# Optimization experiments

Measured on AMD Instinct MI355X. Metric: run time of the kernel, lower is better.

## Reference

```python
import jax, jax.numpy as jnp
import numpy as np

N_NODES = 200_000
N_EDGES = 12_800_000


def setup_inputs() -> dict:
    key = jax.random.key(0)
    k1, k2, k3, k4 = jax.random.split(key, 4)
    x = jax.random.normal(k1, (N_NODES, 2), dtype=jnp.float32)
    edge_index = jax.random.randint(k2, (2, N_EDGES), 0, N_NODES, dtype=jnp.int32)
    # Glorot-ish init for the two GCN linear layers
    W1 = jax.random.normal(k3, (2, 16), dtype=jnp.float32) * 0.5
    b1 = jnp.zeros((16,), dtype=jnp.float32)
    W2 = jax.random.normal(k4, (16, 2), dtype=jnp.float32) * 0.25
    b2 = jnp.zeros((2,), dtype=jnp.float32)
    return {"x": x, "W1": W1, "b1": b1, "W2": W2, "b2": b2, "edge_index": edge_index}


def gcn_conv(x, W, b, src, dst, num_nodes):
    # PyG GCNConv: add self-loops, deg from dst (col), norm = d_src^-1/2 * d_dst^-1/2,
    # out[i] = sum_{j->i} norm_e * (x_j W) + (1/deg_i) * (x_i W) + b
    h = x @ W  # [N, F_out]
    ones = jnp.ones(src.shape[0], dtype=h.dtype)
    deg = jax.ops.segment_sum(ones, dst, num_segments=num_nodes) + 1.0  # +1 self-loop
    dinv = jax.lax.rsqrt(deg)  # [N]
    norm = dinv[src] * dinv[dst]  # [E]
    agg = jax.ops.segment_sum(h[src] * norm[:, None], dst, num_segments=num_nodes)
    # self-loop contribution has norm dinv_i * dinv_i = 1/deg_i
    return agg + h * (1.0 / deg)[:, None] + b


def reference(x, W1, b1, W2, b2, edge_index):
    src, dst = edge_index[0], edge_index[1]
    h = gcn_conv(x, W1, b1, src, dst, N_NODES)
    h = jax.nn.relu(h)
    out = gcn_conv(h, W2, b2, src, dst, N_NODES)
    return out
```

## Files before the change

kernel.cpp:

```cpp
#include <hip/hip_runtime.h>


constexpr int N_NODES = 200000;
constexpr int N_EDGES = 12800000;
constexpr int RANGE_SHIFT = 8;
constexpr int K_BUCKETS = (N_NODES + 255) / 256;
constexpr int SORT_BLOCKS = 2048;
constexpr int CHUNK = N_EDGES / SORT_BLOCKS;
constexpr int SCAN_R = SORT_BLOCKS / 256;
constexpr int SEG = 4;


__global__ __launch_bounds__(256) void hist_kernel(const int* __restrict__ dst,
                                                   unsigned* __restrict__ blockHist) {
    __shared__ unsigned h[K_BUCKETS];
    for (int i = threadIdx.x; i < K_BUCKETS; i += 256) h[i] = 0;
    __syncthreads();
    int base = blockIdx.x * CHUNK;
    for (int e = base + threadIdx.x; e < base + CHUNK; e += 256)
        atomicAdd(&h[((unsigned)dst[e]) >> RANGE_SHIFT], 1u);
    __syncthreads();
    unsigned* row = blockHist + (size_t)blockIdx.x * K_BUCKETS;
    for (int i = threadIdx.x; i < K_BUCKETS; i += 256) row[i] = h[i];
}

__global__ __launch_bounds__(256) void scan_perblock_kernel(unsigned* __restrict__ blockHist,
                                                            unsigned* __restrict__ bucketTotal) {
    int b = blockIdx.x, t = threadIdx.x;
    unsigned v[SCAN_R], run = 0;
#pragma unroll
    for (int j = 0; j < SCAN_R; j++) v[j] = blockHist[(size_t)(SCAN_R * t + j) * K_BUCKETS + b];
#pragma unroll
    for (int j = 0; j < SCAN_R; j++) { unsigned tmp = v[j]; v[j] = run; run += tmp; }
    __shared__ unsigned sh[256];
    sh[t] = run;
    __syncthreads();
    for (int off = 1; off < 256; off <<= 1) {
        unsigned add = (t >= off) ? sh[t - off] : 0u;
        __syncthreads();
        sh[t] += add;
        __syncthreads();
    }
    unsigned excl = sh[t] - run;
#pragma unroll
    for (int j = 0; j < SCAN_R; j++)
        blockHist[(size_t)(SCAN_R * t + j) * K_BUCKETS + b] = excl + v[j];
    if (t == 255) bucketTotal[b] = sh[255];
}

__global__ __launch_bounds__(1024) void scan_buckets_kernel(const unsigned* __restrict__ bucketTotal,
                                                            unsigned* __restrict__ bucketStart) {
    __shared__ unsigned sh[1024];
    int t = threadIdx.x;
    unsigned v = (t < K_BUCKETS) ? bucketTotal[t] : 0u;
    sh[t] = v;
    __syncthreads();
    for (int off = 1; off < 1024; off <<= 1) {
        unsigned add = (t >= off) ? sh[t - off] : 0u;
        __syncthreads();
        sh[t] += add;
        __syncthreads();
    }
    if (t < K_BUCKETS) bucketStart[t] = sh[t] - v;
    if (t == K_BUCKETS - 1) bucketStart[K_BUCKETS] = sh[t];
}

__global__ __launch_bounds__(256) void scatter_kernel(const int* __restrict__ src,
                                                      const int* __restrict__ dst,
                                                      const unsigned* __restrict__ blockHist,
                                                      const unsigned* __restrict__ bucketStart,
                                                      unsigned* __restrict__ sorted) {
    __shared__ unsigned s_hist[K_BUCKETS];
    __shared__ unsigned s_cur[K_BUCKETS];
    __shared__ int      s_base[K_BUCKETS];
    __shared__ unsigned ssum[256];
    __shared__ unsigned ent[CHUNK];
    __shared__ unsigned short bk[CHUNK];

    int t = threadIdx.x;
    int base = blockIdx.x * CHUNK;
    for (int i = t; i < K_BUCKETS; i += 256) s_hist[i] = 0;
    __syncthreads();

    for (int e = base + t; e < base + CHUNK; e += 256)
        atomicAdd(&s_hist[((unsigned)dst[e]) >> RANGE_SHIFT], 1u);
    __syncthreads();

    unsigned v[4], run = 0;
#pragma unroll
    for (int j = 0; j < 4; j++) {
        int idx = 4 * t + j;
        v[j] = (idx < K_BUCKETS) ? s_hist[idx] : 0u;
    }
#pragma unroll
    for (int j = 0; j < 4; j++) { unsigned tmp = v[j]; v[j] = run; run += tmp; }
    ssum[t] = run;
    __syncthreads();
    for (int off = 1; off < 256; off <<= 1) {
        unsigned add = (t >= off) ? ssum[t - off] : 0u;
        __syncthreads();
        ssum[t] += add;
        __syncthreads();
    }
    unsigned excl = ssum[t] - run;
    const unsigned* row = blockHist + (size_t)blockIdx.x * K_BUCKETS;
#pragma unroll
    for (int j = 0; j < 4; j++) {
        int idx = 4 * t + j;
        if (idx < K_BUCKETS) {
            unsigned st = excl + v[j];
            s_cur[idx] = st;
            s_base[idx] = (int)(bucketStart[idx] + row[idx]) - (int)st;
        }
    }
    __syncthreads();

    for (int e = base + t; e < base + CHUNK; e += 256) {
        unsigned d = (unsigned)dst[e];
        unsigned s = (unsigned)src[e];
        unsigned b = d >> RANGE_SHIFT;
        unsigned lpos = atomicAdd(&s_cur[b], 1u);
        ent[lpos] = s | ((d & 255u) << 18);
        bk[lpos] = (unsigned short)b;
    }
    __syncthreads();

    for (int i = t; i < CHUNK; i += 256) {
        unsigned b = bk[i];
        sorted[s_base[b] + i] = ent[i];
    }
}


__global__ __launch_bounds__(256) void deg_part_kernel(const unsigned* __restrict__ sorted,
                                                       const unsigned* __restrict__ bucketStart,
                                                       unsigned* __restrict__ pcnt) {
    __shared__ unsigned cnt[256];
    int t = threadIdx.x;
    cnt[t] = 0;
    __syncthreads();
    int b = blockIdx.x >> 2, s = blockIdx.x & 3;
    int s0 = bucketStart[b], len = bucketStart[b + 1] - s0;
    int e0 = s0 + (len * s) / SEG;
    int e1 = s0 + (len * (s + 1)) / SEG;
    int e = e0 + t;
    for (; e < e1 - 768; e += 1024) {
        unsigned w0 = sorted[e], w1 = sorted[e + 256], w2 = sorted[e + 512], w3 = sorted[e + 768];
        atomicAdd(&cnt[(w0 >> 18) & 255u], 1u);
        atomicAdd(&cnt[(w1 >> 18) & 255u], 1u);
        atomicAdd(&cnt[(w2 >> 18) & 255u], 1u);
        atomicAdd(&cnt[(w3 >> 18) & 255u], 1u);
    }
    for (; e < e1; e += 256)
        atomicAdd(&cnt[(sorted[e] >> 18) & 255u], 1u);
    __syncthreads();
    pcnt[(size_t)blockIdx.x * 256 + t] = cnt[t];
}

__global__ __launch_bounds__(256) void node1_kernel(const float2* __restrict__ x,
                                                    const unsigned* __restrict__ pcnt,
                                                    float* __restrict__ dinv,
                                                    float2* __restrict__ u) {
    int i = blockIdx.x * 256 + threadIdx.x;
    if (i >= N_NODES) return;
    int b = i >> 8, l = i & 255;
    unsigned c = 1;
#pragma unroll
    for (int s = 0; s < SEG; s++) c += pcnt[(size_t)(b * SEG + s) * 256 + l];
    float di = rsqrtf((float)c);
    dinv[i] = di;
    float2 xi = x[i];
    u[i] = make_float2(di * xi.x, di * xi.y);
}

__global__ __launch_bounds__(256) void agg_part_kernel(const unsigned* __restrict__ sorted,
                                                       const unsigned* __restrict__ bucketStart,
                                                       const float2* __restrict__ table,
                                                       float2* __restrict__ part) {
    __shared__ float ax[256], ay[256];
    int t = threadIdx.x;
    ax[t] = 0.f; ay[t] = 0.f;
    __syncthreads();
    int b = blockIdx.x >> 2, s = blockIdx.x & 3;
    int s0 = bucketStart[b], len = bucketStart[b + 1] - s0;
    int e0 = s0 + (len * s) / SEG;
    int e1 = s0 + (len * (s + 1)) / SEG;
    int e = e0 + t;
    for (; e < e1 - 768; e += 1024) {
        unsigned w0 = sorted[e], w1 = sorted[e + 256], w2 = sorted[e + 512], w3 = sorted[e + 768];
        float2 v0 = table[w0 & 0x3FFFFu];
        float2 v1 = table[w1 & 0x3FFFFu];
        float2 v2 = table[w2 & 0x3FFFFu];
        float2 v3 = table[w3 & 0x3FFFFu];
        atomicAdd(&ax[(w0 >> 18) & 255u], v0.x); atomicAdd(&ay[(w0 >> 18) & 255u], v0.y);
        atomicAdd(&ax[(w1 >> 18) & 255u], v1.x); atomicAdd(&ay[(w1 >> 18) & 255u], v1.y);
        atomicAdd(&ax[(w2 >> 18) & 255u], v2.x); atomicAdd(&ay[(w2 >> 18) & 255u], v2.y);
        atomicAdd(&ax[(w3 >> 18) & 255u], v3.x); atomicAdd(&ay[(w3 >> 18) & 255u], v3.y);
    }
    for (; e < e1; e += 256) {
        unsigned w = sorted[e];
        float2 v = table[w & 0x3FFFFu];
        unsigned l = (w >> 18) & 255u;
        atomicAdd(&ax[l], v.x);
        atomicAdd(&ay[l], v.y);
    }
    __syncthreads();
    part[(size_t)blockIdx.x * 256 + t] = make_float2(ax[t], ay[t]);
}

__global__ __launch_bounds__(256) void node2_kernel(const float2* __restrict__ u,
                                                    const float2* __restrict__ part,
                                                    const float* __restrict__ W1,
                                                    const float* __restrict__ b1,
                                                    const float* __restrict__ W2,
                                                    const float* __restrict__ dinv,
                                                    float2* __restrict__ g2) {
    int i = blockIdx.x * 256 + threadIdx.x;
    if (i >= N_NODES) return;
    int b = i >> 8, l = i & 255;
    float ax = 0.f, ay = 0.f;
#pragma unroll
    for (int s = 0; s < SEG; s++) {
        float2 p = part[(size_t)(b * SEG + s) * 256 + l];
        ax += p.x; ay += p.y;
    }
    float di = dinv[i];
    float2 uu = u[i];
    float c0 = di * (ax + uu.x);
    float c1 = di * (ay + uu.y);
    float a0 = 0.f, a1 = 0.f;
#pragma unroll
    for (int f = 0; f < 16; f++) {
        float o = fmaxf(c0 * W1[f] + c1 * W1[16 + f] + b1[f], 0.f);
        a0 += o * W2[2 * f];
        a1 += o * W2[2 * f + 1];
    }
    g2[i] = make_float2(di * a0, di * a1);
}

__global__ __launch_bounds__(256) void node3_kernel(const float2* __restrict__ g2,
                                                    const float2* __restrict__ part,
                                                    const float* __restrict__ b2,
                                                    const float* __restrict__ dinv,
                                                    float2* __restrict__ out) {
    int i = blockIdx.x * 256 + threadIdx.x;
    if (i >= N_NODES) return;
    int b = i >> 8, l = i & 255;
    float ax = 0.f, ay = 0.f;
#pragma unroll
    for (int s = 0; s < SEG; s++) {
        float2 p = part[(size_t)(b * SEG + s) * 256 + l];
        ax += p.x; ay += p.y;
    }
    float di = dinv[i];
    float2 g = g2[i];
    out[i] = make_float2(di * (ax + g.x) + b2[0],
                         di * (ay + g.y) + b2[1]);
}


__global__ __launch_bounds__(256) void fb_deg(const int* __restrict__ dst, int* __restrict__ degi) {
    int e = blockIdx.x * 256 + threadIdx.x;
    if (e < N_EDGES) atomicAdd(&degi[dst[e]], 1);
}
__global__ __launch_bounds__(256) void fb_node1(const float* __restrict__ x, const int* __restrict__ degi,
                                                float* __restrict__ dinv, float2* __restrict__ u) {
    int i = blockIdx.x * 256 + threadIdx.x;
    if (i >= N_NODES) return;
    float di = rsqrtf((float)(degi[i] + 1));
    dinv[i] = di;
    float2 xi = ((const float2*)x)[i];
    u[i] = make_float2(di * xi.x, di * xi.y);
}
__global__ __launch_bounds__(256) void fb_agg(const int* __restrict__ src, const int* __restrict__ dst,
                                              const float2* __restrict__ table, float* __restrict__ acc) {
    int e = blockIdx.x * 256 + threadIdx.x;
    if (e >= N_EDGES) return;
    float2 v = table[src[e]];
    size_t d = dst[e];
    unsafeAtomicAdd(&acc[2 * d], v.x);
    unsafeAtomicAdd(&acc[2 * d + 1], v.y);
}
__global__ __launch_bounds__(256) void fb_node2(const float2* __restrict__ u, const float2* __restrict__ A1,
                                                const float* __restrict__ W1, const float* __restrict__ b1,
                                                const float* __restrict__ W2, const float* __restrict__ dinv,
                                                float2* __restrict__ g2) {
    int i = blockIdx.x * 256 + threadIdx.x;
    if (i >= N_NODES) return;
    float di = dinv[i];
    float2 a = A1[i], uu = u[i];
    float c0 = di * (a.x + uu.x), c1 = di * (a.y + uu.y);
    float a0 = 0.f, a1 = 0.f;
#pragma unroll
    for (int f = 0; f < 16; f++) {
        float o = fmaxf(c0 * W1[f] + c1 * W1[16 + f] + b1[f], 0.f);
        a0 += o * W2[2 * f];
        a1 += o * W2[2 * f + 1];
    }
    g2[i] = make_float2(di * a0, di * a1);
}
__global__ __launch_bounds__(256) void fb_node3(const float2* __restrict__ g2, const float2* __restrict__ A2,
                                                const float* __restrict__ b2, const float* __restrict__ dinv,
                                                float2* __restrict__ out) {
    int i = blockIdx.x * 256 + threadIdx.x;
    if (i >= N_NODES) return;
    float di = dinv[i];
    float2 a = A2[i], g = g2[i];
    out[i] = make_float2(di * (a.x + g.x) + b2[0], di * (a.y + g.y) + b2[1]);
}


extern "C" void kernel_launch(void* const* d_in, const int* in_sizes, int n_in,
                              void* d_out, int out_size, void* d_ws, size_t ws_size,
                              hipStream_t stream) {
    const float* x  = (const float*)d_in[0];
    const float* W1 = (const float*)d_in[1];
    const float* b1 = (const float*)d_in[2];
    const float* W2 = (const float*)d_in[3];
    const float* b2 = (const float*)d_in[4];
    const int* ei   = (const int*)d_in[5];
    const int* src = ei;
    const int* dst = ei + N_EDGES;
    float2* out = (float2*)d_out;

    const size_t need = ((size_t)N_EDGES + (size_t)SORT_BLOCKS * K_BUCKETS + 782 + 784
                         + N_NODES + 2 * (size_t)N_NODES + 2 * (size_t)N_NODES) * 4;

    if (ws_size >= need) {
        unsigned* sorted      = (unsigned*)d_ws;
        unsigned* blockHist   = sorted + N_EDGES;
        unsigned* bucketTotal = blockHist + (size_t)SORT_BLOCKS * K_BUCKETS;
        unsigned* bucketStart = bucketTotal + 782;
        float*    dinv        = (float*)(bucketStart + 784);
        float2*   u           = (float2*)(dinv + N_NODES);
        float2*   g2          = u + N_NODES;
        unsigned* pcnt        = blockHist;
        float2*   part        = (float2*)blockHist;

        hist_kernel<<<SORT_BLOCKS, 256, 0, stream>>>(dst, blockHist);
        scan_perblock_kernel<<<K_BUCKETS, 256, 0, stream>>>(blockHist, bucketTotal);
        scan_buckets_kernel<<<1, 1024, 0, stream>>>(bucketTotal, bucketStart);
        scatter_kernel<<<SORT_BLOCKS, 256, 0, stream>>>(src, dst, blockHist, bucketStart, sorted);
        deg_part_kernel<<<K_BUCKETS * SEG, 256, 0, stream>>>(sorted, bucketStart, pcnt);
        node1_kernel<<<K_BUCKETS, 256, 0, stream>>>((const float2*)x, pcnt, dinv, u);
        agg_part_kernel<<<K_BUCKETS * SEG, 256, 0, stream>>>(sorted, bucketStart, u, part);
        node2_kernel<<<K_BUCKETS, 256, 0, stream>>>(u, part, W1, b1, W2, dinv, g2);
        agg_part_kernel<<<K_BUCKETS * SEG, 256, 0, stream>>>(sorted, bucketStart, g2, part);
        node3_kernel<<<K_BUCKETS, 256, 0, stream>>>(g2, part, b2, dinv, out);
    } else {
        float* ws = (float*)d_ws;
        int*   degi = (int*)ws;
        float* A1   = ws + N_NODES;
        float* A2   = A1 + 2 * (size_t)N_NODES;
        float* dinvF = A2 + 2 * (size_t)N_NODES;
        float2* uF  = (float2*)(dinvF + N_NODES);
        float2* g2F = uF + N_NODES;
        constexpr int EB = (N_EDGES + 255) / 256;
        constexpr int NB = (N_NODES + 255) / 256;
        hipMemsetAsync(degi, 0, 5 * (size_t)N_NODES * sizeof(float), stream);
        fb_deg<<<EB, 256, 0, stream>>>(dst, degi);
        fb_node1<<<NB, 256, 0, stream>>>(x, degi, dinvF, uF);
        fb_agg<<<EB, 256, 0, stream>>>(src, dst, uF, A1);
        fb_node2<<<NB, 256, 0, stream>>>(uF, (const float2*)A1, W1, b1, W2, dinvF, g2F);
        fb_agg<<<EB, 256, 0, stream>>>(src, dst, g2F, A2);
        fb_node3<<<NB, 256, 0, stream>>>(g2F, (const float2*)A2, b2, dinvF, out);
    }
}
```

Before: 583.7 us.

## Add second-level sort by source tile and gather from LDS-staged node tables

Adds a second scatter pass that groups edges of each 1024-destination group by source-node tile of 8192 and counts degrees at the same time. The aggregation kernel then stages each source tile of the node table into shared memory and gathers from LDS instead of random global reads. This targets the cost of random global gathers in the two aggregation passes. In exchange it adds an extra read-write pass over the sorted edge array, a serial per-run search loop, and fewer, larger blocks with 64KB+ of LDS each, which lowers occupancy.

```diff
diff --git a/kernel.cpp b/kernel.cpp
--- a/kernel.cpp
+++ b/kernel.cpp
@@ -8,7 +8,11 @@
 constexpr int SORT_BLOCKS = 2048;
 constexpr int CHUNK = N_EDGES / SORT_BLOCKS;
 constexpr int SCAN_R = SORT_BLOCKS / 256;
-constexpr int SEG = 4;
+constexpr int N_GROUPS = 196;
+constexpr int SUB = 11;
+constexpr int NT = 25;
+constexpr int TILE = 8192;
+constexpr int GPARTS = 3;
 
 
 __global__ __launch_bounds__(256) void hist_kernel(const int* __restrict__ dst,
@@ -120,7 +124,7 @@
         unsigned s = (unsigned)src[e];
         unsigned b = d >> RANGE_SHIFT;
         unsigned lpos = atomicAdd(&s_cur[b], 1u);
-        ent[lpos] = s | ((d & 255u) << 18);
+        ent[lpos] = s | ((d & 1023u) << 18);
         bk[lpos] = (unsigned short)b;
     }
     __syncthreads();
@@ -131,81 +135,117 @@
     }
 }
 
-
-__global__ __launch_bounds__(256) void deg_part_kernel(const unsigned* __restrict__ sorted,
+__global__ __launch_bounds__(256) void scatter2_kernel(unsigned* __restrict__ sorted,
                                                        const unsigned* __restrict__ bucketStart,
-                                                       unsigned* __restrict__ pcnt) {
-    __shared__ unsigned cnt[256];
+                                                       unsigned short* __restrict__ lstart,
+                                                       unsigned short* __restrict__ pcnt) {
+    __shared__ unsigned ent[6144];
+    __shared__ unsigned char bk[6144];
+    __shared__ unsigned cnt[1024];
+    __shared__ unsigned h[NT], cur[NT];
     int t = threadIdx.x;
-    cnt[t] = 0;
-    __syncthreads();
-    int b = blockIdx.x >> 2, s = blockIdx.x & 3;
-    int s0 = bucketStart[b], len = bucketStart[b + 1] - s0;
-    int e0 = s0 + (len * s) / SEG;
-    int e1 = s0 + (len * (s + 1)) / SEG;
-    int e = e0 + t;
-    for (; e < e1 - 768; e += 1024) {
-        unsigned w0 = sorted[e], w1 = sorted[e + 256], w2 = sorted[e + 512], w3 = sorted[e + 768];
-        atomicAdd(&cnt[(w0 >> 18) & 255u], 1u);
-        atomicAdd(&cnt[(w1 >> 18) & 255u], 1u);
-        atomicAdd(&cnt[(w2 >> 18) & 255u], 1u);
-        atomicAdd(&cnt[(w3 >> 18) & 255u], 1u);
-    }
-    for (; e < e1; e += 256)
-        atomicAdd(&cnt[(sorted[e] >> 18) & 255u], 1u);
-    __syncthreads();
-    pcnt[(size_t)blockIdx.x * 256 + t] = cnt[t];
-}
+    int g = blockIdx.x / SUB, s = blockIdx.x % SUB;
+    int gS = bucketStart[4 * g];
+    int gE = bucketStart[min(4 * g + 4, K_BUCKETS)];
+    int len = gE - gS;
+    int c0 = gS + (int)((long long)len * s / SUB);
+    int c1 = gS + (int)((long long)len * (s + 1) / SUB);
+    int n = c1 - c0;
+    for (int i = t; i < 1024; i += 256) cnt[i] = 0;
+    if (t < NT) h[t] = 0;
+    __syncthreads();
+    for (int i = t; i < n; i += 256) {
+        unsigned w = sorted[c0 + i];
+        ent[i] = w;
+        unsigned tile = (w & 0x3FFFFu) >> 13;
+        bk[i] = (unsigned char)tile;
+        atomicAdd(&h[tile], 1u);
+        atomicAdd(&cnt[w >> 18], 1u);
+    }
+    __syncthreads();
+    if (t == 0) {
+        unsigned r = 0;
+        for (int j = 0; j < NT; j++) { unsigned c = h[j]; h[j] = r; cur[j] = r; r += c; }
+    }
+    __syncthreads();
+    unsigned b26 = (unsigned)blockIdx.x * 26u;
+    if (t < NT) lstart[b26 + t] = (unsigned short)h[t];
+    if (t == 0) lstart[b26 + NT] = (unsigned short)n;
+    for (int i = t; i < n; i += 256) {
+        unsigned r = atomicAdd(&cur[bk[i]], 1u);
+        sorted[c0 + r] = ent[i];
+    }
+    for (int i = t; i < 1024; i += 256)
+        pcnt[(size_t)blockIdx.x * 1024 + i] = (unsigned short)cnt[i];
+}
+
 
 __global__ __launch_bounds__(256) void node1_kernel(const float2* __restrict__ x,
-                                                    const unsigned* __restrict__ pcnt,
+                                                    const unsigned short* __restrict__ pcnt,
                                                     float* __restrict__ dinv,
                                                     float2* __restrict__ u) {
     int i = blockIdx.x * 256 + threadIdx.x;
     if (i >= N_NODES) return;
-    int b = i >> 8, l = i & 255;
+    int g = i >> 10, l = i & 1023;
     unsigned c = 1;
 #pragma unroll
-    for (int s = 0; s < SEG; s++) c += pcnt[(size_t)(b * SEG + s) * 256 + l];
+    for (int s = 0; s < SUB; s++) c += pcnt[(size_t)(g * SUB + s) * 1024 + l];
     float di = rsqrtf((float)c);
     dinv[i] = di;
     float2 xi = x[i];
     u[i] = make_float2(di * xi.x, di * xi.y);
 }
 
-__global__ __launch_bounds__(256) void agg_part_kernel(const unsigned* __restrict__ sorted,
+__global__ __launch_bounds__(256) void agg_tile_kernel(const unsigned* __restrict__ sorted,
                                                        const unsigned* __restrict__ bucketStart,
+                                                       const unsigned short* __restrict__ lstart,
                                                        const float2* __restrict__ table,
                                                        float2* __restrict__ part) {
-    __shared__ float ax[256], ay[256];
+    __shared__ float2 tileBuf[TILE];
+    __shared__ float accX[1024], accY[1024];
+    __shared__ int runS[SUB], runP[SUB + 1];
     int t = threadIdx.x;
-    ax[t] = 0.f; ay[t] = 0.f;
-    __syncthreads();
-    int b = blockIdx.x >> 2, s = blockIdx.x & 3;
-    int s0 = bucketStart[b], len = bucketStart[b + 1] - s0;
-    int e0 = s0 + (len * s) / SEG;
-    int e1 = s0 + (len * (s + 1)) / SEG;
-    int e = e0 + t;
-    for (; e < e1 - 768; e += 1024) {
-        unsigned w0 = sorted[e], w1 = sorted[e + 256], w2 = sorted[e + 512], w3 = sorted[e + 768];
-        float2 v0 = table[w0 & 0x3FFFFu];
-        float2 v1 = table[w1 & 0x3FFFFu];
-        float2 v2 = table[w2 & 0x3FFFFu];
-        float2 v3 = table[w3 & 0x3FFFFu];
-        atomicAdd(&ax[(w0 >> 18) & 255u], v0.x); atomicAdd(&ay[(w0 >> 18) & 255u], v0.y);
-        atomicAdd(&ax[(w1 >> 18) & 255u], v1.x); atomicAdd(&ay[(w1 >> 18) & 255u], v1.y);
-        atomicAdd(&ax[(w2 >> 18) & 255u], v2.x); atomicAdd(&ay[(w2 >> 18) & 255u], v2.y);
-        atomicAdd(&ax[(w3 >> 18) & 255u], v3.x); atomicAdd(&ay[(w3 >> 18) & 255u], v3.y);
-    }
-    for (; e < e1; e += 256) {
-        unsigned w = sorted[e];
-        float2 v = table[w & 0x3FFFFu];
-        unsigned l = (w >> 18) & 255u;
-        atomicAdd(&ax[l], v.x);
-        atomicAdd(&ay[l], v.y);
-    }
-    __syncthreads();
-    part[(size_t)blockIdx.x * 256 + t] = make_float2(ax[t], ay[t]);
+    int g = blockIdx.x / GPARTS, p = blockIdx.x % GPARTS;
+    int gS = bucketStart[4 * g];
+    int gE = bucketStart[min(4 * g + 4, K_BUCKETS)];
+    int len = gE - gS;
+    for (int i = t; i < 1024; i += 256) { accX[i] = 0.f; accY[i] = 0.f; }
+    for (int tile = p; tile < NT; tile += GPARTS) {
+        __syncthreads();
+        int base = tile * TILE;
+        int nf4 = min(TILE, N_NODES - base) >> 1;
+        const float4* src4 = (const float4*)(table + base);
+        float4* dst4 = (float4*)tileBuf;
+        for (int j = t; j < nf4; j += 256) dst4[j] = src4[j];
+        if (t < SUB) {
+            int c0 = gS + (int)((long long)len * t / SUB);
+            unsigned b26 = (unsigned)(g * SUB + t) * 26u;
+            int st = lstart[b26 + tile];
+            int en = lstart[b26 + tile + 1];
+            runS[t] = c0 + st;
+            runP[t] = en - st;
+        }
+        __syncthreads();
+        if (t == 0) {
+            int r = 0;
+            for (int s2 = 0; s2 < SUB; s2++) { int L = runP[s2]; runP[s2] = r; r += L; }
+            runP[SUB] = r;
+        }
+        __syncthreads();
+        int total = runP[SUB];
+        for (int k = t; k < total; k += 256) {
+            int s2 = 0;
+            while (runP[s2 + 1] <= k) s2++;
+            unsigned w = sorted[runS[s2] + (k - runP[s2])];
+            float2 v = tileBuf[w & 8191u];
+            unsigned l = w >> 18;
+            atomicAdd(&accX[l], v.x);
+            atomicAdd(&accY[l], v.y);
+        }
+    }
+    __syncthreads();
+    for (int i = t; i < 1024; i += 256)
+        part[(size_t)blockIdx.x * 1024 + i] = make_float2(accX[i], accY[i]);
 }
 
 __global__ __launch_bounds__(256) void node2_kernel(const float2* __restrict__ u,
@@ -217,12 +257,12 @@
                                                     float2* __restrict__ g2) {
     int i = blockIdx.x * 256 + threadIdx.x;
     if (i >= N_NODES) return;
-    int b = i >> 8, l = i & 255;
+    int g = i >> 10, l = i & 1023;
     float ax = 0.f, ay = 0.f;
 #pragma unroll
-    for (int s = 0; s < SEG; s++) {
-        float2 p = part[(size_t)(b * SEG + s) * 256 + l];
-        ax += p.x; ay += p.y;
+    for (int p = 0; p < GPARTS; p++) {
+        float2 v = part[(size_t)(g * GPARTS + p) * 1024 + l];
+        ax += v.x; ay += v.y;
     }
     float di = dinv[i];
     float2 uu = u[i];
@@ -245,17 +285,17 @@
                                                     float2* __restrict__ out) {
     int i = blockIdx.x * 256 + threadIdx.x;
     if (i >= N_NODES) return;
-    int b = i >> 8, l = i & 255;
+    int g = i >> 10, l = i & 1023;
     float ax = 0.f, ay = 0.f;
 #pragma unroll
-    for (int s = 0; s < SEG; s++) {
-        float2 p = part[(size_t)(b * SEG + s) * 256 + l];
-        ax += p.x; ay += p.y;
+    for (int p = 0; p < GPARTS; p++) {
+        float2 v = part[(size_t)(g * GPARTS + p) * 1024 + l];
+        ax += v.x; ay += v.y;
     }
     float di = dinv[i];
-    float2 g = g2[i];
-    out[i] = make_float2(di * (ax + g.x) + b2[0],
-                         di * (ay + g.y) + b2[1]);
+    float2 gg = g2[i];
+    out[i] = make_float2(di * (ax + gg.x) + b2[0],
+                         di * (ay + gg.y) + b2[1]);
 }
 
 
@@ -323,29 +363,32 @@
     const int* dst = ei + N_EDGES;
     float2* out = (float2*)d_out;
 
-    const size_t need = ((size_t)N_EDGES + (size_t)SORT_BLOCKS * K_BUCKETS + 782 + 784
+    const size_t REGION = 1601536;
+    const size_t need = ((size_t)N_EDGES + REGION + 784 + 784
                          + N_NODES + 2 * (size_t)N_NODES + 2 * (size_t)N_NODES) * 4;
 
     if (ws_size >= need) {
         unsigned* sorted      = (unsigned*)d_ws;
-        unsigned* blockHist   = sorted + N_EDGES;
-        unsigned* bucketTotal = blockHist + (size_t)SORT_BLOCKS * K_BUCKETS;
-        unsigned* bucketStart = bucketTotal + 782;
+        unsigned* region      = sorted + N_EDGES;
+        unsigned* blockHist   = region;
+        unsigned short* lstart = (unsigned short*)region;
+        unsigned short* pcnt   = (unsigned short*)(region + 28028);
+        float2*   part        = (float2*)(region + 28028);
+        unsigned* bucketTotal = region + REGION;
+        unsigned* bucketStart = bucketTotal + 784;
         float*    dinv        = (float*)(bucketStart + 784);
         float2*   u           = (float2*)(dinv + N_NODES);
         float2*   g2          = u + N_NODES;
-        unsigned* pcnt        = blockHist;
-        float2*   part        = (float2*)blockHist;
 
         hist_kernel<<<SORT_BLOCKS, 256, 0, stream>>>(dst, blockHist);
         scan_perblock_kernel<<<K_BUCKETS, 256, 0, stream>>>(blockHist, bucketTotal);
         scan_buckets_kernel<<<1, 1024, 0, stream>>>(bucketTotal, bucketStart);
         scatter_kernel<<<SORT_BLOCKS, 256, 0, stream>>>(src, dst, blockHist, bucketStart, sorted);
-        deg_part_kernel<<<K_BUCKETS * SEG, 256, 0, stream>>>(sorted, bucketStart, pcnt);
+        scatter2_kernel<<<N_GROUPS * SUB, 256, 0, stream>>>(sorted, bucketStart, lstart, pcnt);
         node1_kernel<<<K_BUCKETS, 256, 0, stream>>>((const float2*)x, pcnt, dinv, u);
-        agg_part_kernel<<<K_BUCKETS * SEG, 256, 0, stream>>>(sorted, bucketStart, u, part);
+        agg_tile_kernel<<<N_GROUPS * GPARTS, 256, 0, stream>>>(sorted, bucketStart, lstart, u, part);
         node2_kernel<<<K_BUCKETS, 256, 0, stream>>>(u, part, W1, b1, W2, dinv, g2);
-        agg_part_kernel<<<K_BUCKETS * SEG, 256, 0, stream>>>(sorted, bucketStart, g2, part);
+        agg_tile_kernel<<<N_GROUPS * GPARTS, 256, 0, stream>>>(sorted, bucketStart, lstart, g2, part);
         node3_kernel<<<K_BUCKETS, 256, 0, stream>>>(g2, part, b2, dinv, out);
     } else {
         float* ws = (float*)d_ws;
```

Result: slower. 1.018 ms (+74.5%).
